# Kernel tuning notes

Hardware: AMD Instinct MI355X
Metric: run time of the kernel (lower is better)

## Reference

```python
import jax, jax.numpy as jnp
import numpy as np

BETA = 5.5  # exp-kernel sharpness (DualMem.beta)


def _l2norm(x, axis=-1, eps=0.0):
    return x / jnp.linalg.norm(x, axis=axis, keepdims=True)


def setup_inputs() -> dict:
    key = jax.random.key(0)
    k1, k2 = jax.random.split(key)
    B, C, M, D = 64, 1000, 11, 1024
    # CLIP-style unit-norm features (the module asserts/assumes normalized feats)
    img = _l2norm(jax.random.normal(k1, (B, D), dtype=jnp.float32))
    mem = _l2norm(jax.random.normal(k2, (C, M, D), dtype=jnp.float32))
    return {"img_features": img, "memorized_image_feat": mem}


def reference(img_features, memorized_image_feat):
    # Faithful translation of DualMem.fast_get_image_pred:
    #   sim[b,c,m]  = <img[b], mem[c,m]>
    #   w           = exp(-beta * (1 - sim))          (exp-kernel, NOT softmax)
    #   adapt[b,c]  = sum_m mem[c,m] * w[b,c,m]
    #   adapt       = adapt / ||adapt||
    #   logits[b,c] = 100 * <img[b], adapt[b,c]>
    sim = jnp.einsum('bd,cmd->bcm', img_features, memorized_image_feat)
    w = jnp.exp(-BETA * (1.0 - sim))  # [B,C,M]
    adapt = jnp.einsum('cmd,bcm->bcd', memorized_image_feat, w)  # [B,C,D]
    adapt = adapt / jnp.linalg.norm(adapt, axis=-1, keepdims=True)
    logits = 100.0 * jnp.einsum('bd,bcd->bc', img_features, adapt)  # [B,C]
    return logits
```

## Files before the change

### kernel.cpp

```cpp
#include <hip/hip_runtime.h>
#include <hip/hip_bf16.h>


constexpr int Bn = 64;
constexpr int Cn = 1000;
constexpr int Mn = 11;
constexpr int Dn = 1024;
constexpr int LSTR = 516;
constexpr float BETA = 5.5f;

typedef __attribute__((ext_vector_type(8))) short bf16x8;
typedef __attribute__((ext_vector_type(4))) float f32x4;

__device__ inline short f2bf(float x) {
    union { __hip_bfloat16 h; short s; } u;
    u.h = __float2bfloat16(x);
    return u.s;
}

__device__ inline bf16x8 pack_bf16x8(const float4 a, const float4 b) {
    bf16x8 r;
    r[0] = f2bf(a.x); r[1] = f2bf(a.y); r[2] = f2bf(a.z); r[3] = f2bf(a.w);
    r[4] = f2bf(b.x); r[5] = f2bf(b.y); r[6] = f2bf(b.z); r[7] = f2bf(b.w);
    return r;
}

__global__ __launch_bounds__(256) void pack_img_kernel(
    const float* __restrict__ img, bf16x8* __restrict__ imgP) {
    const int t = blockIdx.x * 256 + threadIdx.x;
    const int l = t & 63;
    const int kstep = (t >> 6) & 31;
    const int w = t >> 11;
    const int row = w * 16 + (l & 15);
    const int kcol = kstep * 32 + (l >> 4) * 8;
    const float4 a0 = *reinterpret_cast<const float4*>(img + row * Dn + kcol);
    const float4 a1 = *reinterpret_cast<const float4*>(img + row * Dn + kcol + 4);
    imgP[t] = pack_bf16x8(a0, a1);
}

__global__ __launch_bounds__(256) void fused5_kernel(
    const bf16x8* __restrict__ imgP, const float* __restrict__ mem,
    float* __restrict__ out) {
    __shared__ float arena[Mn * LSTR];
    float* memL  = arena;
    float* redS  = arena;
    f32x4* redGp = (f32x4*)(arena + 3072);
    float* redG  = arena + 3072 + 256 * 4;

    const int c   = blockIdx.x;
    const int tid = threadIdx.x;
    const int l   = tid & 63;
    const int w   = tid >> 6;
    const int rw  = l & 15;
    const int mrow = (rw < Mn) ? rw : 0;
    const int kb   = (l >> 4) * 8;

    const float* mc = mem + (size_t)c * (Mn * Dn);

    f32x4 sS0 = {0.f,0.f,0.f,0.f}, sS1 = {0.f,0.f,0.f,0.f};
    f32x4 sS2 = {0.f,0.f,0.f,0.f}, sS3 = {0.f,0.f,0.f,0.f};
    f32x4 gA  = {0.f,0.f,0.f,0.f};

#pragma unroll
    for (int kq = 0; kq < 2; ++kq) {
        if (kq) __syncthreads();
        for (int u = tid; u < Mn * 128; u += 256) {
            const int row = u >> 7;
            const int c4  = (u & 127) * 4;
            const float4 v = *reinterpret_cast<const float4*>(
                mc + row * Dn + kq * 512 + c4);
            *reinterpret_cast<float4*>(&memL[row * LSTR + c4]) = v;
        }
        __syncthreads();
#pragma unroll
        for (int j = 0; j < 4; ++j) {
            const int ks = 4 * w + j;
            const int kstep = 16 * kq + ks;
            const float4 m0 = *reinterpret_cast<const float4*>(
                &memL[mrow * LSTR + ks * 32 + kb]);
            const float4 m1 = *reinterpret_cast<const float4*>(
                &memL[mrow * LSTR + ks * 32 + kb + 4]);
            const bf16x8 f = pack_bf16x8(m0, m1);
            gA = __builtin_amdgcn_mfma_f32_16x16x32_bf16(f, f, gA, 0, 0, 0);
            const bf16x8* p = imgP + kstep * 64 + l;
            const bf16x8 a0 = p[0];
            const bf16x8 a1 = p[2048];
            const bf16x8 a2 = p[4096];
            const bf16x8 a3 = p[6144];
            sS0 = __builtin_amdgcn_mfma_f32_16x16x32_bf16(a0, f, sS0, 0, 0, 0);
            sS1 = __builtin_amdgcn_mfma_f32_16x16x32_bf16(a1, f, sS1, 0, 0, 0);
            sS2 = __builtin_amdgcn_mfma_f32_16x16x32_bf16(a2, f, sS2, 0, 0, 0);
            sS3 = __builtin_amdgcn_mfma_f32_16x16x32_bf16(a3, f, sS3, 0, 0, 0);
        }
    }
    __syncthreads();

    const int mcol = l & 15;
    const int r0   = (l >> 4) * 4;
    if (mcol < Mn) {
#pragma unroll
        for (int q = 0; q < 4; ++q) {
            redS[(w * 64 +  0 + r0 + q) * 12 + mcol] = sS0[q];
            redS[(w * 64 + 16 + r0 + q) * 12 + mcol] = sS1[q];
            redS[(w * 64 + 32 + r0 + q) * 12 + mcol] = sS2[q];
            redS[(w * 64 + 48 + r0 + q) * 12 + mcol] = sS3[q];
        }
    }
    redGp[w * 64 + l] = gA;
    __syncthreads();

    if (tid < 64) {
        const f32x4 g = redGp[0 * 64 + l] + redGp[1 * 64 + l]
                      + redGp[2 * 64 + l] + redGp[3 * 64 + l];
        if (mcol < Mn) {
            if (r0 + 0 < Mn) redG[(r0 + 0) * Mn + mcol] = g[0];
            if (r0 + 1 < Mn) redG[(r0 + 1) * Mn + mcol] = g[1];
            if (r0 + 2 < Mn) redG[(r0 + 2) * Mn + mcol] = g[2];
            if (r0 + 3 < Mn) redG[(r0 + 3) * Mn + mcol] = g[3];
        }
    }
    __syncthreads();

    if (tid < Bn) {
        const int b = tid;
        float wv[Mn];
        float numer = 0.f;
#pragma unroll
        for (int m = 0; m < Mn; ++m) {
            const float s = redS[(0 * 64 + b) * 12 + m]
                          + redS[(1 * 64 + b) * 12 + m]
                          + redS[(2 * 64 + b) * 12 + m]
                          + redS[(3 * 64 + b) * 12 + m];
            wv[m] = __expf(BETA * (s - 1.f));
            numer = fmaf(wv[m], s, numer);
        }
        float den2 = 0.f;
#pragma unroll
        for (int i = 0; i < Mn; ++i) {
            float row = 0.f;
#pragma unroll
            for (int j = 0; j < Mn; ++j) row = fmaf(wv[j], redG[i * Mn + j], row);
            den2 = fmaf(wv[i], row, den2);
        }
        out[b * Cn + c] = 100.f * numer / sqrtf(den2);
    }
}

__global__ __launch_bounds__(256) void fused2_kernel(
    const float* __restrict__ img, const float* __restrict__ mem,
    float* __restrict__ out) {
    __shared__ float redS[4][Bn][12];
    __shared__ f32x4 redGp[4][64];
    __shared__ float redG[Mn * Mn];

    const int c   = blockIdx.x;
    const int tid = threadIdx.x;
    const int l   = tid & 63;
    const int w   = tid >> 6;
    const int rw  = l & 15;
    const int mrow = (rw < Mn) ? rw : 0;
    const int kb   = (l >> 4) * 8;

    const float* mc = mem + (size_t)c * (Mn * Dn) + mrow * Dn + kb;

    f32x4 accS0 = {0.f,0.f,0.f,0.f}, accS1 = {0.f,0.f,0.f,0.f};
    f32x4 accS2 = {0.f,0.f,0.f,0.f}, accS3 = {0.f,0.f,0.f,0.f};
    f32x4 accG  = {0.f,0.f,0.f,0.f};

#pragma unroll
    for (int j = 0; j < 8; ++j) {
        const int kstep = 8 * w + j;
        const float4 m0 = *reinterpret_cast<const float4*>(mc + kstep * 32);
        const float4 m1 = *reinterpret_cast<const float4*>(mc + kstep * 32 + 4);
        const bf16x8 f = pack_bf16x8(m0, m1);
        accG = __builtin_amdgcn_mfma_f32_16x16x32_bf16(f, f, accG, 0, 0, 0);
        const float* ic = img + rw * Dn + kstep * 32 + kb;
        const float4 i00 = *reinterpret_cast<const float4*>(ic);
        const float4 i01 = *reinterpret_cast<const float4*>(ic + 4);
        const float4 i10 = *reinterpret_cast<const float4*>(ic + 16 * Dn);
        const float4 i11 = *reinterpret_cast<const float4*>(ic + 16 * Dn + 4);
        const float4 i20 = *reinterpret_cast<const float4*>(ic + 32 * Dn);
        const float4 i21 = *reinterpret_cast<const float4*>(ic + 32 * Dn + 4);
        const float4 i30 = *reinterpret_cast<const float4*>(ic + 48 * Dn);
        const float4 i31 = *reinterpret_cast<const float4*>(ic + 48 * Dn + 4);
        const bf16x8 a0 = pack_bf16x8(i00, i01);
        const bf16x8 a1 = pack_bf16x8(i10, i11);
        const bf16x8 a2 = pack_bf16x8(i20, i21);
        const bf16x8 a3 = pack_bf16x8(i30, i31);
        accS0 = __builtin_amdgcn_mfma_f32_16x16x32_bf16(a0, f, accS0, 0, 0, 0);
        accS1 = __builtin_amdgcn_mfma_f32_16x16x32_bf16(a1, f, accS1, 0, 0, 0);
        accS2 = __builtin_amdgcn_mfma_f32_16x16x32_bf16(a2, f, accS2, 0, 0, 0);
        accS3 = __builtin_amdgcn_mfma_f32_16x16x32_bf16(a3, f, accS3, 0, 0, 0);
    }

    const int mcol = l & 15;
    const int r0   = (l >> 4) * 4;
    if (mcol < Mn) {
#pragma unroll
        for (int q = 0; q < 4; ++q) {
            redS[w][ 0 + r0 + q][mcol] = accS0[q];
            redS[w][16 + r0 + q][mcol] = accS1[q];
            redS[w][32 + r0 + q][mcol] = accS2[q];
            redS[w][48 + r0 + q][mcol] = accS3[q];
        }
    }
    redGp[w][l] = accG;
    __syncthreads();

    if (tid < 64) {
        const f32x4 g = redGp[0][l] + redGp[1][l] + redGp[2][l] + redGp[3][l];
        if (mcol < Mn) {
            if (r0 + 0 < Mn) redG[(r0 + 0) * Mn + mcol] = g[0];
            if (r0 + 1 < Mn) redG[(r0 + 1) * Mn + mcol] = g[1];
            if (r0 + 2 < Mn) redG[(r0 + 2) * Mn + mcol] = g[2];
            if (r0 + 3 < Mn) redG[(r0 + 3) * Mn + mcol] = g[3];
        }
    }
    __syncthreads();

    if (tid < Bn) {
        const int b = tid;
        float wv[Mn];
        float numer = 0.f;
#pragma unroll
        for (int m = 0; m < Mn; ++m) {
            const float s = redS[0][b][m] + redS[1][b][m]
                          + redS[2][b][m] + redS[3][b][m];
            wv[m] = __expf(BETA * (s - 1.f));
            numer = fmaf(wv[m], s, numer);
        }
        float den2 = 0.f;
#pragma unroll
        for (int i = 0; i < Mn; ++i) {
            float row = 0.f;
#pragma unroll
            for (int j = 0; j < Mn; ++j) row = fmaf(wv[j], redG[i * Mn + j], row);
            den2 = fmaf(wv[i], row, den2);
        }
        out[b * Cn + c] = 100.f * numer / sqrtf(den2);
    }
}

extern "C" void kernel_launch(void* const* d_in, const int* in_sizes, int n_in,
                              void* d_out, int out_size, void* d_ws, size_t ws_size,
                              hipStream_t stream) {
    const float* img = (const float*)d_in[0];
    const float* mem = (const float*)d_in[1];
    float* out = (float*)d_out;
    (void)in_sizes; (void)n_in; (void)out_size;

    constexpr size_t IMGP_B = (size_t)4 * 32 * 64 * 16;

    if (ws_size >= IMGP_B) {
        bf16x8* imgP = (bf16x8*)d_ws;
        pack_img_kernel<<<dim3(32), dim3(256), 0, stream>>>(img, imgP);
        fused5_kernel<<<dim3(Cn), dim3(256), 0, stream>>>(imgP, mem, out);
    } else {
        fused2_kernel<<<dim3(Cn), dim3(256), 0, stream>>>(img, mem, out);
    }
}
```

Before: 22.93 us.

## Split batch across two blocks per class and load memory directly without LDS staging

The fused kernel now launches a 2D grid (class × batch half), so each block computes similarities for 32 images instead of 64, which doubles the block count for better occupancy and latency hiding. Memory features are read straight from global into registers rather than staged through shared memory, which removes the LDS copy and the syncs inside the loop. In exchange, each class's memory rows are read by two blocks and the Gram matrix is computed twice. Uncoalesced-ish direct float4 loads replace the cooperative staging.

```diff
diff --git a/kernel.cpp b/kernel.cpp
--- a/kernel.cpp
+++ b/kernel.cpp
@@ -6,7 +6,6 @@
 constexpr int Cn = 1000;
 constexpr int Mn = 11;
 constexpr int Dn = 1024;
-constexpr int LSTR = 516;
 constexpr float BETA = 5.5f;
 
 typedef __attribute__((ext_vector_type(8))) short bf16x8;
@@ -38,16 +37,15 @@
     imgP[t] = pack_bf16x8(a0, a1);
 }
 
-__global__ __launch_bounds__(256) void fused5_kernel(
+__global__ __launch_bounds__(256) void fused6_kernel(
     const bf16x8* __restrict__ imgP, const float* __restrict__ mem,
     float* __restrict__ out) {
-    __shared__ float arena[Mn * LSTR];
-    float* memL  = arena;
-    float* redS  = arena;
-    f32x4* redGp = (f32x4*)(arena + 3072);
-    float* redG  = arena + 3072 + 256 * 4;
+    __shared__ float redS[4][32][12];
+    __shared__ f32x4 redGp[4][64];
+    __shared__ float redG[Mn * Mn];
 
     const int c   = blockIdx.x;
+    const int bh  = blockIdx.y;
     const int tid = threadIdx.x;
     const int l   = tid & 63;
     const int w   = tid >> 6;
@@ -55,63 +53,41 @@
     const int mrow = (rw < Mn) ? rw : 0;
     const int kb   = (l >> 4) * 8;
 
-    const float* mc = mem + (size_t)c * (Mn * Dn);
-
-    f32x4 sS0 = {0.f,0.f,0.f,0.f}, sS1 = {0.f,0.f,0.f,0.f};
-    f32x4 sS2 = {0.f,0.f,0.f,0.f}, sS3 = {0.f,0.f,0.f,0.f};
+    const float* mc = mem + (size_t)c * (Mn * Dn) + mrow * Dn + kb;
+    const bf16x8* pA0 = imgP + (size_t)(2 * bh + 0) * 2048 + l;
+    const bf16x8* pA1 = imgP + (size_t)(2 * bh + 1) * 2048 + l;
+
+    f32x4 sS0 = {0.f,0.f,0.f,0.f};
+    f32x4 sS1 = {0.f,0.f,0.f,0.f};
     f32x4 gA  = {0.f,0.f,0.f,0.f};
 
 #pragma unroll
-    for (int kq = 0; kq < 2; ++kq) {
-        if (kq) __syncthreads();
-        for (int u = tid; u < Mn * 128; u += 256) {
-            const int row = u >> 7;
-            const int c4  = (u & 127) * 4;
-            const float4 v = *reinterpret_cast<const float4*>(
-                mc + row * Dn + kq * 512 + c4);
-            *reinterpret_cast<float4*>(&memL[row * LSTR + c4]) = v;
-        }
-        __syncthreads();
-#pragma unroll
-        for (int j = 0; j < 4; ++j) {
-            const int ks = 4 * w + j;
-            const int kstep = 16 * kq + ks;
-            const float4 m0 = *reinterpret_cast<const float4*>(
-                &memL[mrow * LSTR + ks * 32 + kb]);
-            const float4 m1 = *reinterpret_cast<const float4*>(
-                &memL[mrow * LSTR + ks * 32 + kb + 4]);
-            const bf16x8 f = pack_bf16x8(m0, m1);
-            gA = __builtin_amdgcn_mfma_f32_16x16x32_bf16(f, f, gA, 0, 0, 0);
-            const bf16x8* p = imgP + kstep * 64 + l;
-            const bf16x8 a0 = p[0];
-            const bf16x8 a1 = p[2048];
-            const bf16x8 a2 = p[4096];
-            const bf16x8 a3 = p[6144];
-            sS0 = __builtin_amdgcn_mfma_f32_16x16x32_bf16(a0, f, sS0, 0, 0, 0);
-            sS1 = __builtin_amdgcn_mfma_f32_16x16x32_bf16(a1, f, sS1, 0, 0, 0);
-            sS2 = __builtin_amdgcn_mfma_f32_16x16x32_bf16(a2, f, sS2, 0, 0, 0);
-            sS3 = __builtin_amdgcn_mfma_f32_16x16x32_bf16(a3, f, sS3, 0, 0, 0);
-        }
-    }
-    __syncthreads();
+    for (int j = 0; j < 8; ++j) {
+        const int kstep = 8 * w + j;
+        const float4 m0 = *reinterpret_cast<const float4*>(mc + kstep * 32);
+        const float4 m1 = *reinterpret_cast<const float4*>(mc + kstep * 32 + 4);
+        const bf16x8 f = pack_bf16x8(m0, m1);
+        gA = __builtin_amdgcn_mfma_f32_16x16x32_bf16(f, f, gA, 0, 0, 0);
+        const bf16x8 a0 = pA0[kstep * 64];
+        const bf16x8 a1 = pA1[kstep * 64];
+        sS0 = __builtin_amdgcn_mfma_f32_16x16x32_bf16(a0, f, sS0, 0, 0, 0);
+        sS1 = __builtin_amdgcn_mfma_f32_16x16x32_bf16(a1, f, sS1, 0, 0, 0);
+    }
 
     const int mcol = l & 15;
     const int r0   = (l >> 4) * 4;
     if (mcol < Mn) {
 #pragma unroll
         for (int q = 0; q < 4; ++q) {
-            redS[(w * 64 +  0 + r0 + q) * 12 + mcol] = sS0[q];
-            redS[(w * 64 + 16 + r0 + q) * 12 + mcol] = sS1[q];
-            redS[(w * 64 + 32 + r0 + q) * 12 + mcol] = sS2[q];
-            redS[(w * 64 + 48 + r0 + q) * 12 + mcol] = sS3[q];
-        }
-    }
-    redGp[w * 64 + l] = gA;
+            redS[w][ 0 + r0 + q][mcol] = sS0[q];
+            redS[w][16 + r0 + q][mcol] = sS1[q];
+        }
+    }
+    redGp[w][l] = gA;
     __syncthreads();
 
     if (tid < 64) {
-        const f32x4 g = redGp[0 * 64 + l] + redGp[1 * 64 + l]
-                      + redGp[2 * 64 + l] + redGp[3 * 64 + l];
+        const f32x4 g = redGp[0][l] + redGp[1][l] + redGp[2][l] + redGp[3][l];
         if (mcol < Mn) {
             if (r0 + 0 < Mn) redG[(r0 + 0) * Mn + mcol] = g[0];
             if (r0 + 1 < Mn) redG[(r0 + 1) * Mn + mcol] = g[1];
@@ -121,16 +97,15 @@
     }
     __syncthreads();
 
-    if (tid < Bn) {
-        const int b = tid;
+    if (tid < 32) {
+        const int bl = tid;
+        const int b  = bh * 32 + bl;
         float wv[Mn];
         float numer = 0.f;
 #pragma unroll
         for (int m = 0; m < Mn; ++m) {
-            const float s = redS[(0 * 64 + b) * 12 + m]
-                          + redS[(1 * 64 + b) * 12 + m]
-                          + redS[(2 * 64 + b) * 12 + m]
-                          + redS[(3 * 64 + b) * 12 + m];
+            const float s = redS[0][bl][m] + redS[1][bl][m]
+                          + redS[2][bl][m] + redS[3][bl][m];
             wv[m] = __expf(BETA * (s - 1.f));
             numer = fmaf(wv[m], s, numer);
         }
@@ -254,7 +229,7 @@
     if (ws_size >= IMGP_B) {
         bf16x8* imgP = (bf16x8*)d_ws;
         pack_img_kernel<<<dim3(32), dim3(256), 0, stream>>>(img, imgP);
-        fused5_kernel<<<dim3(Cn), dim3(256), 0, stream>>>(imgP, mem, out);
+        fused6_kernel<<<dim3(Cn, 2), dim3(256), 0, stream>>>(imgP, mem, out);
     } else {
         fused2_kernel<<<dim3(Cn), dim3(256), 0, stream>>>(img, mem, out);
     }
```

Result: slower. 28.33 us (+23.6%).
